# Optimization experiments

Hardware: AMD Instinct MI355X
Metric: run time of the kernel (lower is better)

The kernel has to match this reference:

```python
import jax, jax.numpy as jnp
import numpy as np
from jax import lax

SIGMA = 1.0          # block_elemnts.combined_sigma
BN_EPS = 1e-5


def setup_inputs() -> dict:
    key = jax.random.key(0)
    k1, k2, k3, k4 = jax.random.split(key, 4)
    B, N, T, C_in, C_out = 8, 1024, 8, 64, 64
    return {
        "points": jax.random.normal(k1, (B, N, 3), dtype=jnp.float32),
        "translations": jax.random.normal(k2, (B, T, 3), dtype=jnp.float32),
        "functions": jax.random.normal(k3, (B, N, C_in), dtype=jnp.float32),
        "k_tensor": jax.random.normal(k4, (C_out, C_in, T), dtype=jnp.float32)
            * np.sqrt(2.0 / (C_in + C_out)),  # xavier_normal_
        "gamma": jnp.ones((C_out,), dtype=jnp.float32),
        "beta": jnp.zeros((C_out,), dtype=jnp.float32),
    }


def reference(points, translations, functions, k_tensor, gamma, beta):
    denom = 2.0 * SIGMA ** 2
    # pairwise squared distances [B,N,N]
    sq = jnp.sum(points * points, axis=-1)                      # [B,N]
    dist = sq[:, :, None] + sq[:, None, :] \
        - 2.0 * jnp.einsum('bnd,bmd->bnm', points, points)      # [B,N,N]
    # interpolation matrix = Gaussian kernel of distances
    interp_rowsum = jnp.sum(jnp.exp(-dist / denom), axis=2, keepdims=True)  # [B,N,1]
    w = functions / interp_rowsum                               # [B,N,Cin]
    # b_tensor[t] = w @ k_tensor[:,:,t]^T  -> [T,B,N,Cout]
    b = jnp.einsum('bnc,oct->tbno', w, k_tensor)
    ptd = jnp.einsum('bnd,btd->tbn', points, translations)      # [T,B,N]
    tsq = jnp.sum(translations * translations, axis=2).T        # [T,B]

    B_, N_, O_ = b.shape[1], b.shape[2], b.shape[3]

    def step(acc, inputs):
        b_t, ptd_t, tsq_t = inputs                              # [B,N,O],[B,N],[B]
        dot = -2.0 * ptd_t                                      # [B,N]
        # exponent = -||p_i - p_j - t||^2 / (2*sigma^2), always <= 0
        q = jnp.exp(-(dist + dot[:, :, None] - dot[:, None, :]
                      + tsq_t[:, None, None]) / denom)          # [B,N,N]
        return acc + jnp.einsum('bnm,bmo->bno', q, b_t), None

    out, _ = lax.scan(step, jnp.zeros((B_, N_, O_), dtype=b.dtype),
                      (b, ptd, tsq))                            # [B,N,O]

    # BatchNorm1d in training mode over (B,N) per channel, then ReLU
    mean = jnp.mean(out, axis=(0, 1))
    var = jnp.var(out, axis=(0, 1))
    xn = (out - mean) * lax.rsqrt(var + BN_EPS) * gamma + beta
    return jax.nn.relu(xn)                                      # [B,N,Cout]
```

## Files before the change

### kernel.cpp

```cpp
#include <hip/hip_runtime.h>
#include <hip/hip_bf16.h>
#include <cstdint>
#include <cstddef>

#define BN_EPS 1e-5f

typedef float f32x4_t __attribute__((ext_vector_type(4)));
typedef __bf16 bf16x8_t __attribute__((ext_vector_type(8)));

__device__ __forceinline__ unsigned short f2bf(float f) {
    __hip_bfloat16 h = __float2bfloat16(f);
    return __builtin_bit_cast(unsigned short, h);
}

__device__ __forceinline__ void gld_lds16(void* lds, const void* gp) {
#if __has_builtin(__builtin_amdgcn_global_load_lds)
    __builtin_amdgcn_global_load_lds(
        (const __attribute__((address_space(1))) unsigned int*)gp,
        (__attribute__((address_space(3))) unsigned int*)lds, 16, 0, 0);
#else
    *(uint4*)lds = *(const uint4*)gp;
#endif
}


__global__ __launch_bounds__(256) void k_g(const float* __restrict__ points,
                                           const float* __restrict__ ktens,
                                           unsigned short* __restrict__ G,
                                           float* __restrict__ rowsum,
                                           unsigned short* __restrict__ kpb,
                                           float* __restrict__ bns) {
    __shared__ float praw[3072];
    __shared__ float px[1024], py[1024], pz[1024], hq[1024];
    __shared__ float rs[8];

    const int tid = threadIdx.x;
    if (blockIdx.x >= 1024) {
        const int i = (blockIdx.x - 1024) * 256 + tid;
        const int t = i >> 12, o = (i >> 6) & 63, c = i & 63;
        kpb[i] = f2bf(ktens[(o * 64 + c) * 8 + t]);
        if (blockIdx.x == 1024 && tid < 128) bns[tid] = 0.f;
        return;
    }

    const int b  = blockIdx.x & 7;
    const int n0 = (blockIdx.x >> 3) * 8;

    for (int i = tid; i < 3072; i += 256) praw[i] = points[b * 3072 + i];
    if (tid < 8) rs[tid] = 0.f;
    __syncthreads();
    for (int n = tid; n < 1024; n += 256) {
        float x = praw[n * 3], y = praw[n * 3 + 1], z = praw[n * 3 + 2];
        px[n] = x; py[n] = y; pz[n] = z;
        hq[n] = -0.5f * (x * x + y * y + z * z);
    }
    __syncthreads();

    const int rhalf = tid >> 7;
    const int c0 = (tid & 127) * 8;
    float vx[8], vy[8], vz[8], vh[8];
    *(float4*)&vx[0] = *(const float4*)&px[c0];
    *(float4*)&vx[4] = *(const float4*)&px[c0 + 4];
    *(float4*)&vy[0] = *(const float4*)&py[c0];
    *(float4*)&vy[4] = *(const float4*)&py[c0 + 4];
    *(float4*)&vz[0] = *(const float4*)&pz[c0];
    *(float4*)&vz[4] = *(const float4*)&pz[c0 + 4];
    *(float4*)&vh[0] = *(const float4*)&hq[c0];
    *(float4*)&vh[4] = *(const float4*)&hq[c0 + 4];

    unsigned short* gb = G + ((size_t)b << 20);

    #pragma unroll
    for (int u = 0; u < 4; ++u) {
        const int rl = u * 2 + rhalf;
        const int row = n0 + rl;
        const float rx = px[row], ry = py[row], rz = pz[row], hr = hq[row];
        unsigned short us[8];
        float ssum = 0.f;
        #pragma unroll
        for (int j = 0; j < 8; ++j) {
            float e = __expf(hr + vh[j] + rx * vx[j] + ry * vy[j] + rz * vz[j]);
            ssum += e;
            us[j] = f2bf(e);
        }
        uint4 pk;
        pk.x = us[0] | ((unsigned int)us[1] << 16);
        pk.y = us[2] | ((unsigned int)us[3] << 16);
        pk.z = us[4] | ((unsigned int)us[5] << 16);
        pk.w = us[6] | ((unsigned int)us[7] << 16);
        *(uint4*)(gb + (size_t)row * 1024 + c0) = pk;
        #pragma unroll
        for (int m = 32; m; m >>= 1) ssum += __shfl_xor(ssum, m, 64);
        if ((tid & 63) == 0) atomicAdd(&rs[rl], ssum);
    }
    __syncthreads();
    if (tid < 8) rowsum[b * 1024 + n0 + tid] = rs[tid];
}

__global__ __launch_bounds__(256) void k_prep(const float* __restrict__ points,
                                              const float* __restrict__ trans,
                                              const float* __restrict__ funcs,
                                              const unsigned short* __restrict__ kpb,
                                              const float* __restrict__ rowsum,
                                              unsigned short* __restrict__ bmatT,
                                              float* __restrict__ escale) {
    __shared__ unsigned short Asm[128 * 72];
    __shared__ unsigned short Bsm[128 * 72];
    __shared__ float sfacl[256];

    const int b  = blockIdx.x & 7;
    const int mt = (blockIdx.x >> 3) & 7;
    const int ct = blockIdx.x >> 6;
    const int m0 = mt * 128;

    const int tid  = threadIdx.x;
    const int wave = tid >> 6, lane = tid & 63;
    const int wr = wave >> 1, wc = wave & 1;
    const int fr = lane & 15, quad = lane >> 4;

    {
        const int tloc = tid >> 7, m = tid & 127;
        const int t = ct * 2 + tloc;
        const float tx = trans[b * 24 + t * 3], ty = trans[b * 24 + t * 3 + 1],
                    tz = trans[b * 24 + t * 3 + 2];
        const float* pp = &points[(size_t)(b * 1024 + m0 + m) * 3];
        const float ptd = pp[0] * tx + pp[1] * ty + pp[2] * tz;
        const float tsq = tx * tx + ty * ty + tz * tz;
        const float rsv = rowsum[b * 1024 + m0 + m];
        sfacl[tloc * 128 + m] = __expf(-ptd - 0.5f * tsq) / rsv;
        escale[(size_t)(b * 8 + t) * 1024 + m0 + m] = __expf(ptd);
    }
    #pragma unroll
    for (int rep = 0; rep < 2; ++rep) {
        const int m = rep * 64 + (tid >> 2);
        const int c16 = (tid & 3) * 16;
        const float* fp = &funcs[((size_t)(b * 1024) + m0 + m) * 64 + c16];
        float4 f0 = *(const float4*)fp, f1 = *(const float4*)(fp + 4);
        float4 f2 = *(const float4*)(fp + 8), f3 = *(const float4*)(fp + 12);
        uint4 p0, p1;
        p0.x = f2bf(f0.x) | ((unsigned)f2bf(f0.y) << 16);
        p0.y = f2bf(f0.z) | ((unsigned)f2bf(f0.w) << 16);
        p0.z = f2bf(f1.x) | ((unsigned)f2bf(f1.y) << 16);
        p0.w = f2bf(f1.z) | ((unsigned)f2bf(f1.w) << 16);
        p1.x = f2bf(f2.x) | ((unsigned)f2bf(f2.y) << 16);
        p1.y = f2bf(f2.z) | ((unsigned)f2bf(f2.w) << 16);
        p1.z = f2bf(f3.x) | ((unsigned)f2bf(f3.y) << 16);
        p1.w = f2bf(f3.z) | ((unsigned)f2bf(f3.w) << 16);
        *(uint4*)&Asm[m * 72 + c16] = p0;
        *(uint4*)&Asm[m * 72 + c16 + 8] = p1;
    }
    #pragma unroll
    for (int rep = 0; rep < 4; ++rep) {
        const int col = rep * 32 + (tid >> 3);
        const int c8 = (tid & 7) * 8;
        uint4 v = *(const uint4*)&kpb[(size_t)(ct * 128 + col) * 64 + c8];
        *(uint4*)&Bsm[col * 72 + c8] = v;
    }
    __syncthreads();

    f32x4_t acc[4][4];
    #pragma unroll
    for (int i = 0; i < 4; ++i)
        #pragma unroll
        for (int j = 0; j < 4; ++j) acc[i][j] = f32x4_t{0.f, 0.f, 0.f, 0.f};

    #pragma unroll
    for (int s = 0; s < 2; ++s) {
        uint4 afr[4], bfr[4];
        #pragma unroll
        for (int i = 0; i < 4; ++i)
            afr[i] = *(const uint4*)&Asm[(wr * 64 + i * 16 + fr) * 72 + s * 32 + quad * 8];
        #pragma unroll
        for (int j = 0; j < 4; ++j)
            bfr[j] = *(const uint4*)&Bsm[(wc * 64 + j * 16 + fr) * 72 + s * 32 + quad * 8];
        #pragma unroll
        for (int i = 0; i < 4; ++i)
            #pragma unroll
            for (int j = 0; j < 4; ++j)
                acc[i][j] = __builtin_amdgcn_mfma_f32_16x16x32_bf16(
                    __builtin_bit_cast(bf16x8_t, afr[i]),
                    __builtin_bit_cast(bf16x8_t, bfr[j]),
                    acc[i][j], 0, 0, 0);
    }

    #pragma unroll
    for (int i = 0; i < 4; ++i) {
        #pragma unroll
        for (int j = 0; j < 4; ++j) {
            const int colg = ct * 128 + wc * 64 + j * 16 + fr;
            ushort4 pk;
            {
                const int mb = wr * 64 + i * 16 + quad * 4;
                pk.x = f2bf(acc[i][j][0] * sfacl[wc * 128 + mb + 0]);
                pk.y = f2bf(acc[i][j][1] * sfacl[wc * 128 + mb + 1]);
                pk.z = f2bf(acc[i][j][2] * sfacl[wc * 128 + mb + 2]);
                pk.w = f2bf(acc[i][j][3] * sfacl[wc * 128 + mb + 3]);
                *(ushort4*)&bmatT[(size_t)(b * 512 + colg) * 1024 + m0 + mb] = pk;
            }
        }
    }
}

__global__ __launch_bounds__(256) void k_gemm(const unsigned short* __restrict__ G,
                                              const unsigned short* __restrict__ bmatT,
                                              const float* __restrict__ escale,
                                              float* __restrict__ He2) {
    __shared__ unsigned short As[4096];
    __shared__ unsigned short Bs[4096];
    __shared__ float escT[1024];
    __shared__ float red[128 * 20];

    const int b  = blockIdx.x & 7;
    const int rt = (blockIdx.x >> 3) & 7;
    const int z  = blockIdx.x >> 6;
    const int og = z & 3;
    const int kh = z >> 2;
    const int n0 = rt * 128;
    const int kb = kh * 256;

    const int tid  = threadIdx.x;
    const int wave = tid >> 6, lane = tid & 63;
    const int wr = wave >> 1, wc = wave & 1;

    {
        const int t = tid >> 5, r4 = (tid & 31) * 4;
        *(float4*)&escT[t * 128 + r4] =
            *(const float4*)&escale[(size_t)(b * 8 + t) * 1024 + n0 + r4];
    }

    const unsigned short* gA = G + ((size_t)b << 20) + (size_t)n0 * 1024 + kb;
    const unsigned short* gB = bmatT + (size_t)(b * 512 + og * 16) * 1024 + kb;

    const int r16 = lane >> 2;
    const int kq  = lane & 3;
    const int gsw = kq ^ (r16 & 3);
    const size_t gAoff = (size_t)r16 * 1024 + gsw * 8;

    f32x4_t acc[4][4];
    #pragma unroll
    for (int i = 0; i < 4; ++i)
        #pragma unroll
        for (int j = 0; j < 4; ++j) acc[i][j] = f32x4_t{0.f, 0.f, 0.f, 0.f};

    const int fr = lane & 15;
    const int swoff = ((lane >> 4) ^ (fr & 3)) << 4;

    for (int kk = 0; kk < 8; ++kk) {
        const int k0 = kk * 32;
        __syncthreads();
        #pragma unroll
        for (int i = 0; i < 2; ++i) {
            const int seg = wave * 2 + i;
            gld_lds16((char*)As + seg * 1024 + lane * 16,
                      gA + (size_t)(seg * 16) * 1024 + k0 + gAoff);
            gld_lds16((char*)Bs + seg * 1024 + lane * 16,
                      gB + (size_t)(seg * 64) * 1024 + (size_t)r16 * 1024 + k0 + gsw * 8);
        }
        __syncthreads();
        uint4 afr[4], bfr[4];
        #pragma unroll
        for (int i = 0; i < 4; ++i)
            afr[i] = *(const uint4*)((const char*)As + (wr * 64 + i * 16 + fr) * 64 + swoff);
        #pragma unroll
        for (int j = 0; j < 4; ++j)
            bfr[j] = *(const uint4*)((const char*)Bs + (wc * 64 + j * 16 + fr) * 64 + swoff);
        #pragma unroll
        for (int i = 0; i < 4; ++i)
            #pragma unroll
            for (int j = 0; j < 4; ++j)
                acc[i][j] = __builtin_amdgcn_mfma_f32_16x16x32_bf16(
                    __builtin_bit_cast(bf16x8_t, afr[i]),
                    __builtin_bit_cast(bf16x8_t, bfr[j]),
                    acc[i][j], 0, 0, 0);
    }

    const int quad = lane >> 4, oo = lane & 15;
    float res[4][4];
    #pragma unroll
    for (int i = 0; i < 4; ++i)
        #pragma unroll
        for (int r = 0; r < 4; ++r) {
            const int lr = wr * 64 + i * 16 + quad * 4 + r;
            float s = 0.f;
            #pragma unroll
            for (int j = 0; j < 4; ++j)
                s += escT[(wc * 4 + j) * 128 + lr] * acc[i][j][r];
            res[i][r] = s;
        }
    if (wc == 0) {
        #pragma unroll
        for (int i = 0; i < 4; ++i)
            #pragma unroll
            for (int r = 0; r < 4; ++r) {
                const int lr = wr * 64 + i * 16 + quad * 4 + r;
                red[lr * 20 + oo] = res[i][r];
            }
    }
    __syncthreads();
    if (wc == 1) {
        #pragma unroll
        for (int i = 0; i < 4; ++i)
            #pragma unroll
            for (int r = 0; r < 4; ++r) {
                const int lr = wr * 64 + i * 16 + quad * 4 + r;
                red[lr * 20 + oo] += res[i][r];
            }
    }
    __syncthreads();
    float* dst = He2 + (size_t)kh * 524288 + (size_t)(b * 1024 + n0) * 64 + og * 16;
    #pragma unroll
    for (int it = 0; it < 2; ++it) {
        const int L = it * 256 + tid;
        const int row = L >> 2, c4 = (L & 3) * 4;
        *(float4*)(dst + (size_t)row * 64 + c4) = *(const float4*)&red[row * 20 + c4];
    }
}

__global__ __launch_bounds__(256) void k_fin(const float* __restrict__ He2,
                                             float* __restrict__ out,
                                             float* __restrict__ bns) {
    __shared__ float s1[16][64], s2[16][64];
    const int tid = threadIdx.x;
    const float4* H4 = (const float4*)He2;
    float a0 = 0.f, a1 = 0.f, a2 = 0.f, a3 = 0.f;
    float q0 = 0.f, q1 = 0.f, q2 = 0.f, q3 = 0.f;
    #pragma unroll
    for (int it = 0; it < 2; ++it) {
        const size_t idx = (size_t)blockIdx.x * 512 + it * 256 + tid;
        float4 s = make_float4(0.f, 0.f, 0.f, 0.f);
        #pragma unroll
        for (int p = 0; p < 4; ++p) {
            float4 h = H4[(size_t)p * 131072 + idx];
            s.x += h.x; s.y += h.y; s.z += h.z; s.w += h.w;
        }
        ((float4*)out)[idx] = s;
        a0 += s.x; a1 += s.y; a2 += s.z; a3 += s.w;
        q0 += s.x * s.x; q1 += s.y * s.y; q2 += s.z * s.z; q3 += s.w * s.w;
    }
    const int g = tid >> 4, o4 = (tid & 15) * 4;
    *(float4*)&s1[g][o4] = make_float4(a0, a1, a2, a3);
    *(float4*)&s2[g][o4] = make_float4(q0, q1, q2, q3);
    __syncthreads();
    if (tid < 64) {
        float sa = 0.f, sb = 0.f;
        #pragma unroll
        for (int r = 0; r < 16; ++r) { sa += s1[r][tid]; sb += s2[r][tid]; }
        atomicAdd(&bns[tid], sa);
        atomicAdd(&bns[64 + tid], sb);
    }
}

__global__ __launch_bounds__(256) void k_bn(float* __restrict__ out,
                                            const float* __restrict__ bns,
                                            const float* __restrict__ gamma,
                                            const float* __restrict__ beta) {
    const int i = blockIdx.x * 256 + threadIdx.x;
    const int o4 = (i & 15) * 4;
    float4 x = ((float4*)out)[i];
    const float4 s  = *(const float4*)&bns[o4];
    const float4 s2 = *(const float4*)&bns[64 + o4];
    const float4 gm = *(const float4*)&gamma[o4];
    const float4 bt = *(const float4*)&beta[o4];
    const float invn = 1.f / 8192.f;
    float m, v, w;
    m = s.x * invn; v = s2.x * invn - m * m; w = __frsqrt_rn(v + BN_EPS) * gm.x;
    x.x = fmaxf((x.x - m) * w + bt.x, 0.f);
    m = s.y * invn; v = s2.y * invn - m * m; w = __frsqrt_rn(v + BN_EPS) * gm.y;
    x.y = fmaxf((x.y - m) * w + bt.y, 0.f);
    m = s.z * invn; v = s2.z * invn - m * m; w = __frsqrt_rn(v + BN_EPS) * gm.z;
    x.z = fmaxf((x.z - m) * w + bt.z, 0.f);
    m = s.w * invn; v = s2.w * invn - m * m; w = __frsqrt_rn(v + BN_EPS) * gm.w;
    x.w = fmaxf((x.w - m) * w + bt.w, 0.f);
    ((float4*)out)[i] = x;
}

extern "C" void kernel_launch(void* const* d_in, const int* in_sizes, int n_in,
                              void* d_out, int out_size, void* d_ws, size_t ws_size,
                              hipStream_t stream) {
    const float* points = (const float*)d_in[0];
    const float* trans  = (const float*)d_in[1];
    const float* funcs  = (const float*)d_in[2];
    const float* ktens  = (const float*)d_in[3];
    const float* gamma  = (const float*)d_in[4];
    const float* beta   = (const float*)d_in[5];
    float* out = (float*)d_out;

    float* ws      = (float*)d_ws;
    float* escale  = ws;
    float* bns     = escale + 65536;
    float* rowsum  = bns + 128;
    float* He2     = rowsum + 8192;
    unsigned short* kpb   = (unsigned short*)(He2 + 2097152);
    unsigned short* G     = kpb + 32768;
    unsigned short* bmatT = G + 8388608;

    k_g<<<1152, 256, 0, stream>>>(points, ktens, G, rowsum, kpb, bns);
    k_prep<<<256, 256, 0, stream>>>(points, trans, funcs, kpb, rowsum, bmatT, escale);
    k_gemm<<<1024, 256, 0, stream>>>(G, bmatT, escale, He2);
    k_fin<<<256, 256, 0, stream>>>(He2, out, bns);
    k_bn<<<512, 256, 0, stream>>>(out, bns, gamma, beta);
}
```

Baseline: 117.7 us.

## Fuse BatchNorm into reduce kernel via grid barrier; widen GEMM K-step to 64

Merges the BN/ReLU kernel into the split-K reduction kernel using an atomic-counter grid barrier, so the output is written once instead of written, re-read and rewritten, and one launch is dropped. Separately, the GEMM now stages 64-wide K tiles with an 8-way XOR swizzle, halving the number of sync'd load phases. It also shares LDS between the tile buffers and the reduction scratch and adds an occupancy hint. The grid barrier depends on all 256 blocks being co-resident, which risks a deadlock if the GPU cannot schedule them all at once.

```diff
diff --git a/kernel.cpp b/kernel.cpp
--- a/kernel.cpp
+++ b/kernel.cpp
@@ -39,7 +39,7 @@
         const int i = (blockIdx.x - 1024) * 256 + tid;
         const int t = i >> 12, o = (i >> 6) & 63, c = i & 63;
         kpb[i] = f2bf(ktens[(o * 64 + c) * 8 + t]);
-        if (blockIdx.x == 1024 && tid < 128) bns[tid] = 0.f;
+        if (blockIdx.x == 1024 && tid < 136) bns[tid] = 0.f;
         return;
     }
 
@@ -201,14 +201,15 @@
     }
 }
 
-__global__ __launch_bounds__(256) void k_gemm(const unsigned short* __restrict__ G,
-                                              const unsigned short* __restrict__ bmatT,
-                                              const float* __restrict__ escale,
-                                              float* __restrict__ He2) {
-    __shared__ unsigned short As[4096];
-    __shared__ unsigned short Bs[4096];
+__global__ __launch_bounds__(256, 4) void k_gemm(const unsigned short* __restrict__ G,
+                                                 const unsigned short* __restrict__ bmatT,
+                                                 const float* __restrict__ escale,
+                                                 float* __restrict__ He2) {
+    __shared__ union {
+        unsigned short AB[2][8192];
+        float red[128 * 20];
+    } sm;
     __shared__ float escT[1024];
-    __shared__ float red[128 * 20];
 
     const int b  = blockIdx.x & 7;
     const int rt = (blockIdx.x >> 3) & 7;
@@ -231,10 +232,9 @@
     const unsigned short* gA = G + ((size_t)b << 20) + (size_t)n0 * 1024 + kb;
     const unsigned short* gB = bmatT + (size_t)(b * 512 + og * 16) * 1024 + kb;
 
-    const int r16 = lane >> 2;
-    const int kq  = lane & 3;
-    const int gsw = kq ^ (r16 & 3);
-    const size_t gAoff = (size_t)r16 * 1024 + gsw * 8;
+    const int r8  = lane >> 3;
+    const int grp = lane & 7;
+    const int gsw = grp ^ r8;
 
     f32x4_t acc[4][4];
     #pragma unroll
@@ -242,39 +242,46 @@
         #pragma unroll
         for (int j = 0; j < 4; ++j) acc[i][j] = f32x4_t{0.f, 0.f, 0.f, 0.f};
 
-    const int fr = lane & 15;
-    const int swoff = ((lane >> 4) ^ (fr & 3)) << 4;
-
-    for (int kk = 0; kk < 8; ++kk) {
-        const int k0 = kk * 32;
+    const int fr = lane & 15, quad = lane >> 4;
+
+    for (int kk = 0; kk < 4; ++kk) {
+        const int k0 = kk * 64;
         __syncthreads();
         #pragma unroll
-        for (int i = 0; i < 2; ++i) {
-            const int seg = wave * 2 + i;
-            gld_lds16((char*)As + seg * 1024 + lane * 16,
-                      gA + (size_t)(seg * 16) * 1024 + k0 + gAoff);
-            gld_lds16((char*)Bs + seg * 1024 + lane * 16,
-                      gB + (size_t)(seg * 64) * 1024 + (size_t)r16 * 1024 + k0 + gsw * 8);
+        for (int i = 0; i < 4; ++i) {
+            const int seg = wave * 4 + i;
+            gld_lds16((char*)sm.AB[0] + seg * 1024 + lane * 16,
+                      gA + (size_t)(seg * 8 + r8) * 1024 + k0 + gsw * 8);
+            const int t8 = seg >> 1, oo0 = (seg & 1) * 8;
+            gld_lds16((char*)sm.AB[1] + seg * 1024 + lane * 16,
+                      gB + (size_t)(t8 * 64 + oo0 + r8) * 1024 + k0 + gsw * 8);
         }
         __syncthreads();
-        uint4 afr[4], bfr[4];
-        #pragma unroll
-        for (int i = 0; i < 4; ++i)
-            afr[i] = *(const uint4*)((const char*)As + (wr * 64 + i * 16 + fr) * 64 + swoff);
-        #pragma unroll
-        for (int j = 0; j < 4; ++j)
-            bfr[j] = *(const uint4*)((const char*)Bs + (wc * 64 + j * 16 + fr) * 64 + swoff);
-        #pragma unroll
-        for (int i = 0; i < 4; ++i)
+        #pragma unroll
+        for (int s = 0; s < 2; ++s) {
+            const int sw = ((s * 4 + quad) ^ (fr & 7)) * 16;
+            uint4 afr[4], bfr[4];
+            #pragma unroll
+            for (int i = 0; i < 4; ++i)
+                afr[i] = *(const uint4*)((const char*)sm.AB[0]
+                         + (wr * 64 + i * 16 + fr) * 128 + sw);
             #pragma unroll
             for (int j = 0; j < 4; ++j)
-                acc[i][j] = __builtin_amdgcn_mfma_f32_16x16x32_bf16(
-                    __builtin_bit_cast(bf16x8_t, afr[i]),
-                    __builtin_bit_cast(bf16x8_t, bfr[j]),
-                    acc[i][j], 0, 0, 0);
-    }
-
-    const int quad = lane >> 4, oo = lane & 15;
+                bfr[j] = *(const uint4*)((const char*)sm.AB[1]
+                         + (wc * 64 + j * 16 + fr) * 128 + sw);
+            #pragma unroll
+            for (int i = 0; i < 4; ++i)
+                #pragma unroll
+                for (int j = 0; j < 4; ++j)
+                    acc[i][j] = __builtin_amdgcn_mfma_f32_16x16x32_bf16(
+                        __builtin_bit_cast(bf16x8_t, afr[i]),
+                        __builtin_bit_cast(bf16x8_t, bfr[j]),
+                        acc[i][j], 0, 0, 0);
+        }
+    }
+    __syncthreads();
+
+    const int oo = lane & 15;
     float res[4][4];
     #pragma unroll
     for (int i = 0; i < 4; ++i)
@@ -293,7 +300,7 @@
             #pragma unroll
             for (int r = 0; r < 4; ++r) {
                 const int lr = wr * 64 + i * 16 + quad * 4 + r;
-                red[lr * 20 + oo] = res[i][r];
+                sm.red[lr * 20 + oo] = res[i][r];
             }
     }
     __syncthreads();
@@ -303,7 +310,7 @@
             #pragma unroll
             for (int r = 0; r < 4; ++r) {
                 const int lr = wr * 64 + i * 16 + quad * 4 + r;
-                red[lr * 20 + oo] += res[i][r];
+                sm.red[lr * 20 + oo] += res[i][r];
             }
     }
     __syncthreads();
@@ -312,16 +319,22 @@
     for (int it = 0; it < 2; ++it) {
         const int L = it * 256 + tid;
         const int row = L >> 2, c4 = (L & 3) * 4;
-        *(float4*)(dst + (size_t)row * 64 + c4) = *(const float4*)&red[row * 20 + c4];
+        *(float4*)(dst + (size_t)row * 64 + c4) = *(const float4*)&sm.red[row * 20 + c4];
     }
 }
 
 __global__ __launch_bounds__(256) void k_fin(const float* __restrict__ He2,
                                              float* __restrict__ out,
-                                             float* __restrict__ bns) {
+                                             float* __restrict__ bns,
+                                             const float* __restrict__ gamma,
+                                             const float* __restrict__ beta) {
     __shared__ float s1[16][64], s2[16][64];
+    __shared__ float bnsl[128];
     const int tid = threadIdx.x;
     const float4* H4 = (const float4*)He2;
+    unsigned int* cnt = (unsigned int*)(bns + 128);
+
+    float4 v[2];
     float a0 = 0.f, a1 = 0.f, a2 = 0.f, a3 = 0.f;
     float q0 = 0.f, q1 = 0.f, q2 = 0.f, q3 = 0.f;
     #pragma unroll
@@ -333,7 +346,7 @@
             float4 h = H4[(size_t)p * 131072 + idx];
             s.x += h.x; s.y += h.y; s.z += h.z; s.w += h.w;
         }
-        ((float4*)out)[idx] = s;
+        v[it] = s;
         a0 += s.x; a1 += s.y; a2 += s.z; a3 += s.w;
         q0 += s.x * s.x; q1 += s.y * s.y; q2 += s.z * s.z; q3 += s.w * s.w;
     }
@@ -348,30 +361,39 @@
         atomicAdd(&bns[tid], sa);
         atomicAdd(&bns[64 + tid], sb);
     }
-}
-
-__global__ __launch_bounds__(256) void k_bn(float* __restrict__ out,
-                                            const float* __restrict__ bns,
-                                            const float* __restrict__ gamma,
-                                            const float* __restrict__ beta) {
-    const int i = blockIdx.x * 256 + threadIdx.x;
-    const int o4 = (i & 15) * 4;
-    float4 x = ((float4*)out)[i];
-    const float4 s  = *(const float4*)&bns[o4];
-    const float4 s2 = *(const float4*)&bns[64 + o4];
-    const float4 gm = *(const float4*)&gamma[o4];
-    const float4 bt = *(const float4*)&beta[o4];
+    __threadfence();
+    __syncthreads();
+    if (tid == 0) {
+        atomicAdd(cnt, 1u);
+        while (__hip_atomic_load(cnt, __ATOMIC_ACQUIRE, __HIP_MEMORY_SCOPE_AGENT) < 256u)
+            __builtin_amdgcn_s_sleep(8);
+    }
+    __syncthreads();
+    if (tid < 128)
+        bnsl[tid] = __hip_atomic_load(&bns[tid], __ATOMIC_RELAXED, __HIP_MEMORY_SCOPE_AGENT);
+    __syncthreads();
+
     const float invn = 1.f / 8192.f;
-    float m, v, w;
-    m = s.x * invn; v = s2.x * invn - m * m; w = __frsqrt_rn(v + BN_EPS) * gm.x;
-    x.x = fmaxf((x.x - m) * w + bt.x, 0.f);
-    m = s.y * invn; v = s2.y * invn - m * m; w = __frsqrt_rn(v + BN_EPS) * gm.y;
-    x.y = fmaxf((x.y - m) * w + bt.y, 0.f);
-    m = s.z * invn; v = s2.z * invn - m * m; w = __frsqrt_rn(v + BN_EPS) * gm.z;
-    x.z = fmaxf((x.z - m) * w + bt.z, 0.f);
-    m = s.w * invn; v = s2.w * invn - m * m; w = __frsqrt_rn(v + BN_EPS) * gm.w;
-    x.w = fmaxf((x.w - m) * w + bt.w, 0.f);
-    ((float4*)out)[i] = x;
+    float mm[4], ww[4], bb[4];
+    #pragma unroll
+    for (int c = 0; c < 4; ++c) {
+        const int ch = o4 + c;
+        const float m = bnsl[ch] * invn;
+        const float var = bnsl[64 + ch] * invn - m * m;
+        mm[c] = m;
+        ww[c] = __frsqrt_rn(var + BN_EPS) * gamma[ch];
+        bb[c] = beta[ch];
+    }
+    #pragma unroll
+    for (int it = 0; it < 2; ++it) {
+        const size_t idx = (size_t)blockIdx.x * 512 + it * 256 + tid;
+        float4 x = v[it];
+        x.x = fmaxf((x.x - mm[0]) * ww[0] + bb[0], 0.f);
+        x.y = fmaxf((x.y - mm[1]) * ww[1] + bb[1], 0.f);
+        x.z = fmaxf((x.z - mm[2]) * ww[2] + bb[2], 0.f);
+        x.w = fmaxf((x.w - mm[3]) * ww[3] + bb[3], 0.f);
+        ((float4*)out)[idx] = x;
+    }
 }
 
 extern "C" void kernel_launch(void* const* d_in, const int* in_sizes, int n_in,
@@ -388,7 +410,7 @@
     float* ws      = (float*)d_ws;
     float* escale  = ws;
     float* bns     = escale + 65536;
-    float* rowsum  = bns + 128;
+    float* rowsum  = bns + 136;
     float* He2     = rowsum + 8192;
     unsigned short* kpb   = (unsigned short*)(He2 + 2097152);
     unsigned short* G     = kpb + 32768;
@@ -397,6 +419,5 @@
     k_g<<<1152, 256, 0, stream>>>(points, ktens, G, rowsum, kpb, bns);
     k_prep<<<256, 256, 0, stream>>>(points, trans, funcs, kpb, rowsum, bmatT, escale);
     k_gemm<<<1024, 256, 0, stream>>>(G, bmatT, escale, He2);
-    k_fin<<<256, 256, 0, stream>>>(He2, out, bns);
-    k_bn<<<512, 256, 0, stream>>>(out, bns, gamma, beta);
-}
+    k_fin<<<256, 256, 0, stream>>>(He2, out, bns, gamma, beta);
+}
```

Result: slower. 139.1 us (+18.1%).

## Retile GEMM waves over full translation dim and drop LDS cross-wave reduction

Applied to the files above, without the earlier changes.

In k_gemm each wave now owns 32 rows and all 8 translation column groups, where before a 2x2 wave grid split the columns. The per-row sum over translations can then be done in registers, which removes the LDS reduction buffer and two barriers. Output is written with scalar stores instead of float4. Separately, the row-sum reduction in k_g replaces shuffle reductions and LDS atomics with a two-level LDS tree. The risks are more B-fragment LDS reads per wave and less coalesced global stores.

```diff
diff --git a/kernel.cpp b/kernel.cpp
--- a/kernel.cpp
+++ b/kernel.cpp
@@ -32,7 +32,8 @@
                                            float* __restrict__ bns) {
     __shared__ float praw[3072];
     __shared__ float px[1024], py[1024], pz[1024], hq[1024];
-    __shared__ float rs[8];
+    __shared__ float part[8][128];
+    __shared__ float p2[8][32];
 
     const int tid = threadIdx.x;
     if (blockIdx.x >= 1024) {
@@ -47,7 +48,6 @@
     const int n0 = (blockIdx.x >> 3) * 8;
 
     for (int i = tid; i < 3072; i += 256) praw[i] = points[b * 3072 + i];
-    if (tid < 8) rs[tid] = 0.f;
     __syncthreads();
     for (int n = tid; n < 1024; n += 256) {
         float x = praw[n * 3], y = praw[n * 3 + 1], z = praw[n * 3 + 2];
@@ -89,12 +89,24 @@
         pk.z = us[4] | ((unsigned int)us[5] << 16);
         pk.w = us[6] | ((unsigned int)us[7] << 16);
         *(uint4*)(gb + (size_t)row * 1024 + c0) = pk;
-        #pragma unroll
-        for (int m = 32; m; m >>= 1) ssum += __shfl_xor(ssum, m, 64);
-        if ((tid & 63) == 0) atomicAdd(&rs[rl], ssum);
-    }
-    __syncthreads();
-    if (tid < 8) rowsum[b * 1024 + n0 + tid] = rs[tid];
+        part[rl][tid & 127] = ssum;
+    }
+    __syncthreads();
+    {
+        const int row = tid >> 5, c4l = (tid & 31) * 4;
+        float4 p = *(const float4*)&part[row][c4l];
+        p2[row][tid & 31] = p.x + p.y + p.z + p.w;
+    }
+    __syncthreads();
+    if (tid < 8) {
+        float s = 0.f;
+        #pragma unroll
+        for (int q = 0; q < 8; ++q) {
+            float4 v = *(const float4*)&p2[tid][q * 4];
+            s += v.x + v.y + v.z + v.w;
+        }
+        rowsum[b * 1024 + n0 + tid] = s;
+    }
 }
 
 __global__ __launch_bounds__(256) void k_prep(const float* __restrict__ points,
@@ -208,7 +220,6 @@
     __shared__ unsigned short As[4096];
     __shared__ unsigned short Bs[4096];
     __shared__ float escT[1024];
-    __shared__ float red[128 * 20];
 
     const int b  = blockIdx.x & 7;
     const int rt = (blockIdx.x >> 3) & 7;
@@ -220,7 +231,6 @@
 
     const int tid  = threadIdx.x;
     const int wave = tid >> 6, lane = tid & 63;
-    const int wr = wave >> 1, wc = wave & 1;
 
     {
         const int t = tid >> 5, r4 = (tid & 31) * 4;
@@ -236,14 +246,15 @@
     const int gsw = kq ^ (r16 & 3);
     const size_t gAoff = (size_t)r16 * 1024 + gsw * 8;
 
-    f32x4_t acc[4][4];
-    #pragma unroll
-    for (int i = 0; i < 4; ++i)
-        #pragma unroll
-        for (int j = 0; j < 4; ++j) acc[i][j] = f32x4_t{0.f, 0.f, 0.f, 0.f};
+    f32x4_t acc[2][8];
+    #pragma unroll
+    for (int i = 0; i < 2; ++i)
+        #pragma unroll
+        for (int j = 0; j < 8; ++j) acc[i][j] = f32x4_t{0.f, 0.f, 0.f, 0.f};
 
     const int fr = lane & 15;
     const int swoff = ((lane >> 4) ^ (fr & 3)) << 4;
+    const int row_base = wave * 32;
 
     for (int kk = 0; kk < 8; ++kk) {
         const int k0 = kk * 32;
@@ -257,62 +268,33 @@
                       gB + (size_t)(seg * 64) * 1024 + (size_t)r16 * 1024 + k0 + gsw * 8);
         }
         __syncthreads();
-        uint4 afr[4], bfr[4];
-        #pragma unroll
-        for (int i = 0; i < 4; ++i)
-            afr[i] = *(const uint4*)((const char*)As + (wr * 64 + i * 16 + fr) * 64 + swoff);
-        #pragma unroll
-        for (int j = 0; j < 4; ++j)
-            bfr[j] = *(const uint4*)((const char*)Bs + (wc * 64 + j * 16 + fr) * 64 + swoff);
-        #pragma unroll
-        for (int i = 0; i < 4; ++i)
-            #pragma unroll
-            for (int j = 0; j < 4; ++j)
-                acc[i][j] = __builtin_amdgcn_mfma_f32_16x16x32_bf16(
-                    __builtin_bit_cast(bf16x8_t, afr[i]),
-                    __builtin_bit_cast(bf16x8_t, bfr[j]),
-                    acc[i][j], 0, 0, 0);
+        uint4 afr0 = *(const uint4*)((const char*)As + (row_base + fr) * 64 + swoff);
+        uint4 afr1 = *(const uint4*)((const char*)As + (row_base + 16 + fr) * 64 + swoff);
+        #pragma unroll
+        for (int j = 0; j < 8; ++j) {
+            uint4 bfr = *(const uint4*)((const char*)Bs + (j * 16 + fr) * 64 + swoff);
+            acc[0][j] = __builtin_amdgcn_mfma_f32_16x16x32_bf16(
+                __builtin_bit_cast(bf16x8_t, afr0),
+                __builtin_bit_cast(bf16x8_t, bfr), acc[0][j], 0, 0, 0);
+            acc[1][j] = __builtin_amdgcn_mfma_f32_16x16x32_bf16(
+                __builtin_bit_cast(bf16x8_t, afr1),
+                __builtin_bit_cast(bf16x8_t, bfr), acc[1][j], 0, 0, 0);
+        }
     }
 
     const int quad = lane >> 4, oo = lane & 15;
-    float res[4][4];
-    #pragma unroll
-    for (int i = 0; i < 4; ++i)
+    float* dst = He2 + (size_t)kh * 524288 + (size_t)(b * 1024 + n0) * 64 + og * 16;
+    #pragma unroll
+    for (int i = 0; i < 2; ++i) {
         #pragma unroll
         for (int r = 0; r < 4; ++r) {
-            const int lr = wr * 64 + i * 16 + quad * 4 + r;
+            const int row = row_base + i * 16 + quad * 4 + r;
             float s = 0.f;
             #pragma unroll
-            for (int j = 0; j < 4; ++j)
-                s += escT[(wc * 4 + j) * 128 + lr] * acc[i][j][r];
-            res[i][r] = s;
-        }
-    if (wc == 0) {
-        #pragma unroll
-        for (int i = 0; i < 4; ++i)
-            #pragma unroll
-            for (int r = 0; r < 4; ++r) {
-                const int lr = wr * 64 + i * 16 + quad * 4 + r;
-                red[lr * 20 + oo] = res[i][r];
-            }
-    }
-    __syncthreads();
-    if (wc == 1) {
-        #pragma unroll
-        for (int i = 0; i < 4; ++i)
-            #pragma unroll
-            for (int r = 0; r < 4; ++r) {
-                const int lr = wr * 64 + i * 16 + quad * 4 + r;
-                red[lr * 20 + oo] += res[i][r];
-            }
-    }
-    __syncthreads();
-    float* dst = He2 + (size_t)kh * 524288 + (size_t)(b * 1024 + n0) * 64 + og * 16;
-    #pragma unroll
-    for (int it = 0; it < 2; ++it) {
-        const int L = it * 256 + tid;
-        const int row = L >> 2, c4 = (L & 3) * 4;
-        *(float4*)(dst + (size_t)row * 64 + c4) = *(const float4*)&red[row * 20 + c4];
+            for (int j = 0; j < 8; ++j)
+                s += escT[j * 128 + row] * acc[i][j][r];
+            dst[(size_t)row * 64 + oo] = s;
+        }
     }
 }
 
```

New measurement: 114.5 us. 1.03x faster.
